# Kernel tuning notes

Measured on AMD Instinct MI355X. Metric: run time of the kernel, lower is better.

The kernel has to match this reference:

```python
import jax, jax.numpy as jnp
import numpy as np

L, D, H, HD, F, V, S, M, B = 8, 1024, 16, 64, 2048, 32000, 1024, 128, 1
EPS = 1e-5

def _rope_tables(total, hd):
    inv = 1.0 / (10000.0 ** (np.arange(0, hd, 2, dtype=np.float64) / hd))
    ang = np.arange(total)[:, None] * inv[None, :]
    cos = np.concatenate([np.cos(ang), np.cos(ang)], -1).astype(np.float32)
    sin = np.concatenate([np.sin(ang), np.sin(ang)], -1).astype(np.float32)
    return jnp.asarray(cos), jnp.asarray(sin)

_COS, _SIN = _rope_tables(M + S + M, HD)
_POS_MEM = jnp.arange(M)
_POS_HID = M + jnp.arange(S)
_POS_BG = M + S + jnp.arange(M)
_kph = jnp.arange(M + S)
# hidden queries: attend to all memory keys + causal over hidden keys
_MASK_H = (_kph[None, :] < M) | (_kph[None, :] - M <= jnp.arange(S)[:, None])
_kpb = jnp.arange(M + S + M)
# beacon/forget queries: attend to all mem+hidden keys + causal over own keys
_MASK_B = (_kpb[None, :] < M + S) | (_kpb[None, :] - (M + S) <= jnp.arange(M)[:, None])


def _rms(x, w):
    return x * w * jax.lax.rsqrt(jnp.mean(x * x, -1, keepdims=True) + EPS)

def _heads(x, w):  # [B,T,D] -> [B,H,T,HD]
    return (x @ w).reshape(B, -1, H, HD).transpose(0, 2, 1, 3)

def _merge(x):  # [B,H,T,HD] -> [B,T,D]
    return x.transpose(0, 2, 1, 3).reshape(B, -1, D)

def _rot_half(x):
    return jnp.concatenate([-x[..., HD // 2:], x[..., :HD // 2]], -1)

def _rope(x, pos):
    return x * _COS[pos][None, None] + _rot_half(x) * _SIN[pos][None, None]

def _attn(q, k, v, mask):
    s = jnp.einsum('bhqd,bhkd->bhqk', q, k) / jnp.sqrt(jnp.float32(HD))
    s = jnp.where(mask[None, None], s, jnp.finfo(s.dtype).min)
    return jnp.einsum('bhqk,bhkd->bhqd', jax.nn.softmax(s, -1), v)


def _forward(input_ids, memory, beacon, forget, embed, ln1, ln2,
             Wq, Wk, Wv, Wo, mWk, mWv, bWq, bWk, bWv, fWq, fWk, fWv, Wg, Wu, Wd):
    hidden = embed[input_ids]  # [B,S,D]

    def step(carry, xs):
        hid, bcn, fgt = carry
        (mem_l, l1, l2, wq, wk, wv, wo, mwk, mwv,
         bwq, bwk, bwv, fwq, fwk, fwv, wg, wu, wd) = xs
        rec = (bcn, fgt)  # states entering the layer (records in torch code)
        cat = jnp.concatenate([hid, bcn, fgt], 1)  # [B,S+2M,D]
        x = _rms(cat, l1)
        hx, bx, fx = x[:, :S], x[:, S:S + M], x[:, S + M:]
        mem = mem_l[None]  # [1,M,D]
        # project_head: memory -> K,V; prepend to hidden KV
        mk = _rope(_heads(mem, mwk), _POS_MEM)
        mv = _heads(mem, mwv)
        qh = _rope(_heads(hx, wq), _POS_HID)
        kh = _rope(_heads(hx, wk), _POS_HID)
        vh = _heads(hx, wv)
        hk = jnp.concatenate([mk, kh], 2)
        hv = jnp.concatenate([mv, vh], 2)
        oh = _merge(_attn(qh, hk, hv, _MASK_H)) @ wo

        def gate_branch(sx, wq_, wk_, wv_):
            q = _rope(_heads(sx, wq_), _POS_BG)
            k = jnp.concatenate([hk, _rope(_heads(sx, wk_), _POS_BG)], 2)
            v = jnp.concatenate([hv, _heads(sx, wv_)], 2)
            return _merge(_attn(q, k, v, _MASK_B)) @ wo

        ob = gate_branch(bx, bwq, bwk, bwv)
        of = gate_branch(fx, fwq, fwk, fwv)
        cat = cat + jnp.concatenate([oh, ob, of], 1)
        y = _rms(cat, l2)
        cat = cat + (jax.nn.silu(y @ wg) * (y @ wu)) @ wd
        return (cat[:, :S], cat[:, S:S + M], cat[:, S + M:]), rec

    xs = (memory, ln1, ln2, Wq, Wk, Wv, Wo, mWk, mWv,
          bWq, bWk, bWv, fWq, fWk, fWv, Wg, Wu, Wd)
    _, (inj, fg) = jax.lax.scan(step, (hidden, beacon, forget), xs)
    inj = inj.reshape(L, M, D)  # B==1
    fg = fg.reshape(L, M, D)
    g = jax.nn.sigmoid(fg)
    return memory * g + inj * (1.0 - g)


def setup_inputs() -> dict:
    key = jax.random.key(0)
    ks = jax.random.split(key, 24)
    sd = jnp.float32(0.02)
    def W(k, shape):
        return jax.random.normal(k, shape, jnp.float32) * sd
    return {
        'input_ids': jax.random.randint(ks[0], (B, S), 0, V),
        'memory': jax.random.normal(ks[1], (L, M, D), jnp.float32),
        'beacon': jax.random.normal(ks[2], (B, M, D), jnp.float32),
        'forget': jax.random.normal(ks[3], (B, M, D), jnp.float32),
        'embed': W(ks[4], (V, D)),
        'ln1': jnp.ones((L, D), jnp.float32),
        'ln2': jnp.ones((L, D), jnp.float32),
        'Wq': W(ks[5], (L, D, D)), 'Wk': W(ks[6], (L, D, D)),
        'Wv': W(ks[7], (L, D, D)), 'Wo': W(ks[8], (L, D, D)),
        'mWk': W(ks[9], (L, D, D)), 'mWv': W(ks[10], (L, D, D)),
        'bWq': W(ks[11], (L, D, D)), 'bWk': W(ks[12], (L, D, D)), 'bWv': W(ks[13], (L, D, D)),
        'fWq': W(ks[14], (L, D, D)), 'fWk': W(ks[15], (L, D, D)), 'fWv': W(ks[16], (L, D, D)),
        'Wg': W(ks[17], (L, D, F)), 'Wu': W(ks[18], (L, D, F)), 'Wd': W(ks[19], (L, F, D)),
    }


def reference(input_ids, memory, beacon, forget, embed, ln1, ln2,
              Wq, Wk, Wv, Wo, mWk, mWv, bWq, bWk, bWv, fWq, fWk, fWv, Wg, Wu, Wd):
    return _forward(input_ids, memory, beacon, forget, embed, ln1, ln2,
                    Wq, Wk, Wv, Wo, mWk, mWv, bWq, bWk, bWv, fWq, fWk, fWv, Wg, Wu, Wd)
```

## Files before the change

### kernel.cpp

```cpp
#include <hip/hip_runtime.h>
#include <math.h>

typedef __bf16 bf16;
typedef __attribute__((ext_vector_type(8))) __bf16 bf16x8;
typedef __attribute__((ext_vector_type(4))) float f32x4;

static const int DM = 1024;
static const int TCAT = 1280;
static const int NKV = 1408;

__device__ inline f32x4 mfma16(bf16x8 a, bf16x8 b, f32x4 c) {
  return __builtin_amdgcn_mfma_f32_16x16x32_bf16(a, b, c, 0, 0, 0);
}

__global__ void rope_table_kernel(float* cosT, float* sinT) {
  int p = blockIdx.x, i = threadIdx.x;
  double freq = pow(10000.0, -((double)i) / 32.0);
  double a = (double)p * freq;
  cosT[p * 32 + i] = (float)cos(a);
  sinT[p * 32 + i] = (float)sin(a);
}

__global__ void init_cat_kernel(const int* ids, const float* embed,
                                const float* beacon, const float* forget,
                                float* cat) {
  int r = blockIdx.x, tid = threadIdx.x;
  const float* src;
  if (r < 1024) src = embed + (size_t)ids[r] * DM;
  else if (r < 1152) src = beacon + (size_t)(r - 1024) * DM;
  else src = forget + (size_t)(r - 1152) * DM;
  *(f32x4*)(cat + (size_t)r * DM + tid * 4) = *(const f32x4*)(src + tid * 4);
}

__global__ void out_gate_kernel(const float* cat, const float* memL, float* outL) {
  int m = blockIdx.x, tid = threadIdx.x;
  size_t c = (size_t)tid * 4;
  f32x4 f = *(const f32x4*)(cat + (size_t)(1152 + m) * DM + c);
  f32x4 j = *(const f32x4*)(cat + (size_t)(1024 + m) * DM + c);
  f32x4 mm = *(const f32x4*)(memL + (size_t)m * DM + c);
  f32x4 o;
#pragma unroll
  for (int r = 0; r < 4; ++r) {
    float g = 1.f / (1.f + __expf(-f[r]));
    o[r] = mm[r] * g + j[r] * (1.f - g);
  }
  *(f32x4*)(outL + (size_t)m * DM + c) = o;
}

struct TransJob { const float* src; bf16* dst; int K; int N; int tileStart; };
struct TransArgs { TransJob j[15]; int njobs; };

__global__ __launch_bounds__(256) void trans_kernel(TransArgs args) {
  int b = blockIdx.x, ji = 0;
  while (ji + 1 < args.njobs && b >= args.j[ji + 1].tileStart) ++ji;
  TransJob J = args.j[ji];
  int t = b - J.tileStart;
  int tilesN = J.N >> 5;
  int tk = t / tilesN, tn = t - tk * tilesN;
  int k0 = tk * 32, n0 = tn * 32;
  __shared__ float tile[32][33];
  int c = threadIdx.x & 31, r0 = threadIdx.x >> 5;
#pragma unroll
  for (int i = 0; i < 4; ++i) {
    int r = r0 + i * 8;
    tile[r][c] = J.src[(size_t)(k0 + r) * J.N + n0 + c];
  }
  __syncthreads();
#pragma unroll
  for (int i = 0; i < 4; ++i) {
    int r = r0 + i * 8;
    J.dst[(size_t)(n0 + r) * J.K + k0 + c] = (bf16)tile[c][r];
  }
}

__global__ __launch_bounds__(256) void rmsnorm_kernel(const float* x, const float* w,
                                                      bf16* out, const float* mem,
                                                      int nNorm) {
  int r = blockIdx.x, tid = threadIdx.x;
  if (r < nNorm) {
    f32x4 v = *(const f32x4*)(x + (size_t)r * DM + tid * 4);
    float ss = v[0] * v[0] + v[1] * v[1] + v[2] * v[2] + v[3] * v[3];
#pragma unroll
    for (int d = 1; d < 64; d <<= 1) ss += __shfl_xor(ss, d, 64);
    __shared__ float red[4];
    if ((tid & 63) == 0) red[tid >> 6] = ss;
    __syncthreads();
    float tot = red[0] + red[1] + red[2] + red[3];
    float scale = rsqrtf(tot * (1.0f / 1024.0f) + 1e-5f);
    f32x4 wv = *(const f32x4*)(w + tid * 4);
    bf16* o = out + (size_t)r * DM + tid * 4;
#pragma unroll
    for (int q = 0; q < 4; ++q) o[q] = (bf16)(v[q] * wv[q] * scale);
  } else {
    f32x4 v = *(const f32x4*)(mem + (size_t)(r - nNorm) * DM + tid * 4);
    bf16* o = out + (size_t)r * DM + tid * 4;
#pragma unroll
    for (int q = 0; q < 4; ++q) o[q] = (bf16)v[q];
  }
}

struct GemmJob { const bf16* A; const bf16* B; float* C; int K; int N; int tileStart; int addFlag; };
struct GemmArgs { GemmJob j[12]; int njobs; };

__device__ __forceinline__ void gll16(const bf16* g, bf16* l) {
  __builtin_amdgcn_global_load_lds(
      (const __attribute__((address_space(1))) void*)g,
      (__attribute__((address_space(3))) void*)l, 16, 0, 0);
}

__global__ __launch_bounds__(256, 2) void gemm_kernel(GemmArgs args) {
  int b = blockIdx.x, ji = 0;
  while (ji + 1 < args.njobs && b >= args.j[ji + 1].tileStart) ++ji;
  GemmJob J = args.j[ji];
  int t = b - J.tileStart;
  int tilesN = J.N >> 7;
  int tm = t / tilesN, tn = t - tm * tilesN;
  const int tid = threadIdx.x;
  const int lane = tid & 63, w = tid >> 6;
  const int l15 = lane & 15, quad = lane >> 4;

  __shared__ bf16 As[2][64 * 32];
  __shared__ bf16 Bs[2][128 * 32];

  f32x4 acc[4][2];
#pragma unroll
  for (int i = 0; i < 4; ++i)
#pragma unroll
    for (int j = 0; j < 2; ++j) acc[i][j] = (f32x4){0.f, 0.f, 0.f, 0.f};

  const bf16* gA  = J.A + (size_t)(tm * 64 + w * 16 + (lane >> 2)) * J.K + (lane & 3) * 8;
  const bf16* gB0 = J.B + (size_t)(tn * 128 + w * 16 + (lane >> 2)) * J.K + (lane & 3) * 8;
  const bf16* gB1 = gB0 + (size_t)64 * J.K;

  auto stage = [&](int buf, int kt) {
    int k0 = kt << 5;
    gll16(gA + k0, &As[buf][w * 512]);
    gll16(gB0 + k0, &Bs[buf][w * 512]);
    gll16(gB1 + k0, &Bs[buf][2048 + w * 512]);
  };

  int nt = J.K >> 5;
  int cur = 0;
  stage(0, 0);
  if (nt > 1) stage(1, 1);

  for (int tt = 0; tt < nt; ++tt) {
    if (tt + 1 < nt) asm volatile("s_waitcnt vmcnt(3)" ::: "memory");
    else             asm volatile("s_waitcnt vmcnt(0)" ::: "memory");
    __builtin_amdgcn_sched_barrier(0);
    __builtin_amdgcn_s_barrier();

    const bf16* Ab = As[cur];
    const bf16* Bb = Bs[cur];
    bf16x8 af[4], bw[2];
#pragma unroll
    for (int i = 0; i < 4; ++i)
      af[i] = *(const bf16x8*)(Ab + (i * 16 + l15) * 32 + quad * 8);
#pragma unroll
    for (int j = 0; j < 2; ++j)
      bw[j] = *(const bf16x8*)(Bb + (w * 32 + j * 16 + l15) * 32 + quad * 8);
    asm volatile("s_waitcnt lgkmcnt(0)" ::: "memory");
    __builtin_amdgcn_sched_barrier(0);
    __builtin_amdgcn_s_barrier();

    if (tt + 2 < nt) stage(cur, tt + 2);

#pragma unroll
    for (int i = 0; i < 4; ++i)
#pragma unroll
      for (int j = 0; j < 2; ++j) acc[i][j] = mfma16(af[i], bw[j], acc[i][j]);
    cur ^= 1;
  }

#pragma unroll
  for (int i = 0; i < 4; ++i)
#pragma unroll
    for (int j = 0; j < 2; ++j) {
      int row0 = tm * 64 + i * 16 + quad * 4;
      int col = tn * 128 + w * 32 + j * 16 + l15;
#pragma unroll
      for (int r = 0; r < 4; ++r) {
        size_t idx = (size_t)(row0 + r) * J.N + col;
        if (J.addFlag) J.C[idx] += acc[i][j][r];
        else J.C[idx] = acc[i][j][r];
      }
    }
}

__global__ __launch_bounds__(256) void rope_vt_kernel(const float* qkv, const float* cosT,
                                                      const float* sinT, bf16* Qb,
                                                      bf16* Kb, bf16* Vt) {
  int b = blockIdx.x;
  if (b < 2688) {
    bool isQ = b < 1280;
    int r = isQ ? b : b - 1280;
    const float* x = qkv + (size_t)(isQ ? r : 1280 + r) * DM;
    int pos = isQ ? (r < 1152 ? r + 128 : r) : (r < 1280 ? r : r - 128);
    bf16* out = (isQ ? Qb : Kb) + (size_t)r * DM;
#pragma unroll
    for (int it = 0; it < 4; ++it) {
      int g = threadIdx.x + it * 256;
      int idx = g & 31;
      float c = cosT[pos * 32 + idx], s = sinT[pos * 32 + idx];
      float xv = x[g];
      float rot = ((g & 63) < 32) ? -x[g + 32] : x[g - 32];
      out[g] = (bf16)(xv * c + rot * s);
    }
  } else {
    int t = b - 2688;
    int tk = t >> 5, td = t & 31;
    int key0 = tk * 32, d0 = td * 32;
    __shared__ float tile[32][33];
    int c = threadIdx.x & 31, r0 = threadIdx.x >> 5;
#pragma unroll
    for (int i = 0; i < 4; ++i) {
      int r = r0 + i * 8;
      tile[r][c] = qkv[(size_t)(2688 + key0 + r) * DM + d0 + c];
    }
    __syncthreads();
#pragma unroll
    for (int i = 0; i < 4; ++i) {
      int r = r0 + i * 8;
      Vt[(size_t)(d0 + r) * NKV + key0 + c] = (bf16)tile[c][r];
    }
  }
}

__global__ __launch_bounds__(64) void attn_kernel(const bf16* Qb, const bf16* Kb,
                                                  const bf16* Vt, bf16* Ob) {
  int b = blockIdx.x;
  int h, q0, qRow0, maskBase, extraOff, kmax;
  if (b < 1024) {
    h = b >> 6; q0 = (b & 63) << 4; qRow0 = 0; maskBase = 128; extraOff = 0;
    kmax = 128 + q0 + 16; if (kmax > 1152) kmax = 1152;
  } else if (b < 1152) {
    int i = b - 1024; h = i >> 3; q0 = (i & 7) << 4; qRow0 = 1024;
    maskBase = 1152; extraOff = 0; kmax = 1152 + q0 + 16;
  } else {
    int i = b - 1152; h = i >> 3; q0 = (i & 7) << 4; qRow0 = 1152;
    maskBase = 1152; extraOff = 128; kmax = 1152 + q0 + 16;
  }
  const int lane = threadIdx.x;
  const int l15 = lane & 15, quad = lane >> 4;
  const bf16* qp = Qb + (size_t)(qRow0 + q0 + l15) * DM + h * 64 + quad * 8;
  bf16x8 aq0 = *(const bf16x8*)qp;
  bf16x8 aq1 = *(const bf16x8*)(qp + 32);
  f32x4 O0 = {0,0,0,0}, O1 = {0,0,0,0}, O2 = {0,0,0,0}, O3 = {0,0,0,0};
  float mrow[4], lrow[4];
#pragma unroll
  for (int r = 0; r < 4; ++r) { mrow[r] = -3.0e38f; lrow[r] = 0.f; }
  __shared__ bf16 Plds[16][32];
  int nkt = (kmax + 31) >> 5;
  for (int kt = 0; kt < nkt; ++kt) {
    int k0 = kt << 5;
    int off = (k0 >= 1152) ? extraOff : 0;
    f32x4 s0 = {0,0,0,0}, s1 = {0,0,0,0};
    {
      const bf16* kp = Kb + (size_t)(k0 + l15 + off) * DM + h * 64 + quad * 8;
      s0 = mfma16(aq0, *(const bf16x8*)kp, s0);
      s0 = mfma16(aq1, *(const bf16x8*)(kp + 32), s0);
      const bf16* kp1 = kp + (size_t)16 * DM;
      s1 = mfma16(aq0, *(const bf16x8*)kp1, s1);
      s1 = mfma16(aq1, *(const bf16x8*)(kp1 + 32), s1);
    }
    float p0[4], p1[4], mt[4];
#pragma unroll
    for (int r = 0; r < 4; ++r) {
      int qi = q0 + quad * 4 + r;
      int key0k = k0 + l15;
      int key1k = key0k + 16;
      float v0 = s0[r] * 0.125f, v1 = s1[r] * 0.125f;
      if (!(key0k < maskBase || key0k - maskBase <= qi)) v0 = -3.0e38f;
      if (!(key1k < maskBase || key1k - maskBase <= qi)) v1 = -3.0e38f;
      p0[r] = v0; p1[r] = v1;
      mt[r] = fmaxf(v0, v1);
    }
#pragma unroll
    for (int d = 1; d < 16; d <<= 1) {
#pragma unroll
      for (int r = 0; r < 4; ++r) mt[r] = fmaxf(mt[r], __shfl_xor(mt[r], d, 64));
    }
    float alpha[4];
#pragma unroll
    for (int r = 0; r < 4; ++r) {
      float mn = fmaxf(mrow[r], mt[r]);
      alpha[r] = __expf(mrow[r] - mn);
      mrow[r] = mn;
      p0[r] = __expf(p0[r] - mn);
      p1[r] = __expf(p1[r] - mn);
    }
    float rs[4];
#pragma unroll
    for (int r = 0; r < 4; ++r) rs[r] = p0[r] + p1[r];
#pragma unroll
    for (int d = 1; d < 16; d <<= 1) {
#pragma unroll
      for (int r = 0; r < 4; ++r) rs[r] += __shfl_xor(rs[r], d, 64);
    }
#pragma unroll
    for (int r = 0; r < 4; ++r) {
      lrow[r] = lrow[r] * alpha[r] + rs[r];
      O0[r] *= alpha[r]; O1[r] *= alpha[r]; O2[r] *= alpha[r]; O3[r] *= alpha[r];
    }
    __syncthreads();
#pragma unroll
    for (int r = 0; r < 4; ++r) {
      Plds[quad * 4 + r][l15] = (bf16)p0[r];
      Plds[quad * 4 + r][l15 + 16] = (bf16)p1[r];
    }
    __syncthreads();
    bf16x8 ap = *(const bf16x8*)(&Plds[l15][quad * 8]);
    const bf16* vp = Vt + (size_t)(h * 64 + l15) * NKV + k0 + off + quad * 8;
    O0 = mfma16(ap, *(const bf16x8*)vp, O0);
    O1 = mfma16(ap, *(const bf16x8*)(vp + (size_t)16 * NKV), O1);
    O2 = mfma16(ap, *(const bf16x8*)(vp + (size_t)32 * NKV), O2);
    O3 = mfma16(ap, *(const bf16x8*)(vp + (size_t)48 * NKV), O3);
  }
#pragma unroll
  for (int r = 0; r < 4; ++r) lrow[r] = 1.0f / lrow[r];
  bf16* op = Ob + (size_t)(qRow0 + q0 + quad * 4) * DM + h * 64 + l15;
#pragma unroll
  for (int r = 0; r < 4; ++r) {
    float inv = lrow[r];
    op[(size_t)r * DM + 0]  = (bf16)(O0[r] * inv);
    op[(size_t)r * DM + 16] = (bf16)(O1[r] * inv);
    op[(size_t)r * DM + 32] = (bf16)(O2[r] * inv);
    op[(size_t)r * DM + 48] = (bf16)(O3[r] * inv);
  }
}

__global__ void silu_kernel(const float* G, const float* U, bf16* H) {
  size_t i = (size_t)blockIdx.x * 256 + threadIdx.x;
  f32x4 g = *(const f32x4*)(G + i * 4);
  f32x4 u = *(const f32x4*)(U + i * 4);
  bf16* o = H + i * 4;
#pragma unroll
  for (int r = 0; r < 4; ++r) {
    float gv = g[r];
    float s = gv / (1.f + __expf(-gv));
    o[r] = (bf16)(s * u[r]);
  }
}

static const size_t OFF_COS = 0;
static const size_t OFF_SIN = 163840;
static const size_t OFF_CAT = 327680;
static const size_t OFF_XB  = 5570560;
static const size_t OFF_QKV = 8454144;
static const size_t OFF_QB  = 25231360;
static const size_t OFF_KB  = 27852800;
static const size_t OFF_VT  = 30736384;
static const size_t OFF_OB  = 33619968;
static const size_t OFF_YB  = 36241408;
static const size_t OFF_WT  = 38862848;
static const size_t OFF_G   = 76611584;
static const size_t OFF_U   = 87097344;
static const size_t OFF_HB  = 97583104;

extern "C" void kernel_launch(void* const* d_in, const int* in_sizes, int n_in,
                              void* d_out, int out_size, void* d_ws, size_t ws_size,
                              hipStream_t stream) {
  const int* ids = (const int*)d_in[0];
  const float* memory = (const float*)d_in[1];
  const float* beacon = (const float*)d_in[2];
  const float* forget = (const float*)d_in[3];
  const float* embed = (const float*)d_in[4];
  const float* ln1 = (const float*)d_in[5];
  const float* ln2 = (const float*)d_in[6];
  const float* Wq = (const float*)d_in[7];
  const float* Wk = (const float*)d_in[8];
  const float* Wv = (const float*)d_in[9];
  const float* Wo = (const float*)d_in[10];
  const float* mWk = (const float*)d_in[11];
  const float* mWv = (const float*)d_in[12];
  const float* bWq = (const float*)d_in[13];
  const float* bWk = (const float*)d_in[14];
  const float* bWv = (const float*)d_in[15];
  const float* fWq = (const float*)d_in[16];
  const float* fWk = (const float*)d_in[17];
  const float* fWv = (const float*)d_in[18];
  const float* Wg = (const float*)d_in[19];
  const float* Wu = (const float*)d_in[20];
  const float* Wd = (const float*)d_in[21];

  char* wsb = (char*)d_ws;
  float* cosT = (float*)(wsb + OFF_COS);
  float* sinT = (float*)(wsb + OFF_SIN);
  float* cat  = (float*)(wsb + OFF_CAT);
  bf16* xb    = (bf16*)(wsb + OFF_XB);
  float* qkv  = (float*)(wsb + OFF_QKV);
  bf16* Qb    = (bf16*)(wsb + OFF_QB);
  bf16* Kb    = (bf16*)(wsb + OFF_KB);
  bf16* Vt    = (bf16*)(wsb + OFF_VT);
  bf16* Ob    = (bf16*)(wsb + OFF_OB);
  bf16* yb    = (bf16*)(wsb + OFF_YB);
  bf16* wt    = (bf16*)(wsb + OFF_WT);
  float* Gf   = (float*)(wsb + OFF_G);
  float* Uf   = (float*)(wsb + OFF_U);
  bf16* Hb    = (bf16*)(wsb + OFF_HB);
  float* outp = (float*)d_out;

  auto mkjob = [](const bf16* A, const bf16* B, float* C, int K, int N, int M,
                  int addFlag, int& tiles) {
    GemmJob j; j.A = A; j.B = B; j.C = C; j.K = K; j.N = N;
    j.tileStart = tiles; j.addFlag = addFlag;
    tiles += (M / 64) * (N / 128);
    return j;
  };

  rope_table_kernel<<<1280, 32, 0, stream>>>(cosT, sinT);
  init_cat_kernel<<<1280, 256, 0, stream>>>(ids, embed, beacon, forget, cat);

  for (int l = 0; l < 8; ++l) {
    out_gate_kernel<<<128, 256, 0, stream>>>(cat, memory + (size_t)l * 131072,
                                             outp + (size_t)l * 131072);
    if (l == 7) break;

    TransArgs ta; int tt = 0;
    const float* s12[12] = {Wq, Wk, Wv, Wo, mWk, mWv, bWq, bWk, bWv, fWq, fWk, fWv};
    for (int i = 0; i < 12; ++i) {
      ta.j[i].src = s12[i] + (size_t)l * 1048576;
      ta.j[i].dst = wt + (size_t)i * 1048576;
      ta.j[i].K = 1024; ta.j[i].N = 1024; ta.j[i].tileStart = tt; tt += 1024;
    }
    ta.j[12].src = Wg + (size_t)l * 2097152; ta.j[12].dst = wt + (size_t)12 * 1048576;
    ta.j[12].K = 1024; ta.j[12].N = 2048; ta.j[12].tileStart = tt; tt += 2048;
    ta.j[13].src = Wu + (size_t)l * 2097152; ta.j[13].dst = wt + (size_t)14 * 1048576;
    ta.j[13].K = 1024; ta.j[13].N = 2048; ta.j[13].tileStart = tt; tt += 2048;
    ta.j[14].src = Wd + (size_t)l * 2097152; ta.j[14].dst = wt + (size_t)16 * 1048576;
    ta.j[14].K = 2048; ta.j[14].N = 1024; ta.j[14].tileStart = tt; tt += 2048;
    ta.njobs = 15;
    trans_kernel<<<tt, 256, 0, stream>>>(ta);

    rmsnorm_kernel<<<1408, 256, 0, stream>>>(cat, ln1 + (size_t)l * 1024, xb,
                                             memory + (size_t)l * 131072, 1280);

    auto xrow = [&](int r) { return xb + (size_t)r * DM; };
    auto crow = [&](int r) { return qkv + (size_t)r * DM; };
    auto wtm = [&](int i) { return wt + (size_t)i * 1048576; };
    GemmArgs ga; int tA = 0; int nj = 0;
    ga.j[nj++] = mkjob(xrow(0),    wtm(0),  crow(0),    1024, 1024, 1024, 0, tA);
    ga.j[nj++] = mkjob(xrow(1024), wtm(6),  crow(1024), 1024, 1024, 128, 0, tA);
    ga.j[nj++] = mkjob(xrow(1152), wtm(9),  crow(1152), 1024, 1024, 128, 0, tA);
    ga.j[nj++] = mkjob(xrow(1280), wtm(4),  crow(1280), 1024, 1024, 128, 0, tA);
    ga.j[nj++] = mkjob(xrow(0),    wtm(1),  crow(1408), 1024, 1024, 1024, 0, tA);
    ga.j[nj++] = mkjob(xrow(1024), wtm(7),  crow(2432), 1024, 1024, 128, 0, tA);
    ga.j[nj++] = mkjob(xrow(1152), wtm(10), crow(2560), 1024, 1024, 128, 0, tA);
    ga.j[nj++] = mkjob(xrow(1280), wtm(5),  crow(2688), 1024, 1024, 128, 0, tA);
    ga.j[nj++] = mkjob(xrow(0),    wtm(2),  crow(2816), 1024, 1024, 1024, 0, tA);
    ga.j[nj++] = mkjob(xrow(1024), wtm(8),  crow(3840), 1024, 1024, 128, 0, tA);
    ga.j[nj++] = mkjob(xrow(1152), wtm(11), crow(3968), 1024, 1024, 128, 0, tA);
    ga.njobs = nj;
    gemm_kernel<<<tA, 256, 0, stream>>>(ga);

    rope_vt_kernel<<<4096, 256, 0, stream>>>(qkv, cosT, sinT, Qb, Kb, Vt);

    attn_kernel<<<1280, 64, 0, stream>>>(Qb, Kb, Vt, Ob);

    GemmArgs gb; int tB = 0;
    gb.j[0] = mkjob(Ob, wtm(3), cat, 1024, 1024, 1280, 1, tB);
    gb.njobs = 1;
    gemm_kernel<<<tB, 256, 0, stream>>>(gb);

    rmsnorm_kernel<<<1280, 256, 0, stream>>>(cat, ln2 + (size_t)l * 1024, yb,
                                             nullptr, 1280);

    GemmArgs gc; int tC = 0;
    gc.j[0] = mkjob(yb, wtm(12), Gf, 1024, 2048, 1280, 0, tC);
    gc.j[1] = mkjob(yb, wtm(14), Uf, 1024, 2048, 1280, 0, tC);
    gc.njobs = 2;
    gemm_kernel<<<tC, 256, 0, stream>>>(gc);

    silu_kernel<<<2560, 256, 0, stream>>>(Gf, Uf, Hb);

    GemmArgs gd; int tD = 0;
    gd.j[0] = mkjob(Hb, wtm(16), cat, 2048, 1024, 1280, 1, tD);
    gd.njobs = 1;
    gemm_kernel<<<tD, 256, 0, stream>>>(gd);
  }
}
```

Before: 1.887 ms.

## Fuse SiLU gating into FFN GEMM, emit V transposed, split-K residual GEMMs

```diff
diff --git a/kernel.cpp b/kernel.cpp
--- a/kernel.cpp
+++ b/kernel.cpp
@@ -99,7 +99,10 @@
   }
 }
 
-struct GemmJob { const bf16* A; const bf16* B; float* C; int K; int N; int tileStart; int addFlag; };
+struct GemmJob {
+  const bf16* A; const bf16* B; const bf16* B2; void* C;
+  int K; int N; int ldC; int tileStart; int nMN; int mode; int kSplit;
+};
 struct GemmArgs { GemmJob j[12]; int njobs; };
 
 __device__ __forceinline__ void gll16(const bf16* g, bf16* l) {
@@ -113,52 +116,77 @@
   while (ji + 1 < args.njobs && b >= args.j[ji + 1].tileStart) ++ji;
   GemmJob J = args.j[ji];
   int t = b - J.tileStart;
+  int ks = 0;
+  if (J.kSplit > 1) { ks = t / J.nMN; t -= ks * J.nMN; }
   int tilesN = J.N >> 7;
   int tm = t / tilesN, tn = t - tm * tilesN;
+  int kLen = J.K / J.kSplit;
+  int kBase = ks * kLen;
   const int tid = threadIdx.x;
   const int lane = tid & 63, w = tid >> 6;
   const int l15 = lane & 15, quad = lane >> 4;
+  const bool ffn = (J.mode == 3);
 
   __shared__ bf16 As[2][64 * 32];
   __shared__ bf16 Bs[2][128 * 32];
-
-  f32x4 acc[4][2];
+  __shared__ bf16 B2s[2][128 * 32];
+
+  f32x4 acc[4][2], acc2[4][2];
 #pragma unroll
   for (int i = 0; i < 4; ++i)
 #pragma unroll
-    for (int j = 0; j < 2; ++j) acc[i][j] = (f32x4){0.f, 0.f, 0.f, 0.f};
-
-  const bf16* gA  = J.A + (size_t)(tm * 64 + w * 16 + (lane >> 2)) * J.K + (lane & 3) * 8;
-  const bf16* gB0 = J.B + (size_t)(tn * 128 + w * 16 + (lane >> 2)) * J.K + (lane & 3) * 8;
+    for (int j = 0; j < 2; ++j) {
+      acc[i][j] = (f32x4){0.f, 0.f, 0.f, 0.f};
+      acc2[i][j] = (f32x4){0.f, 0.f, 0.f, 0.f};
+    }
+
+  const bf16* gA  = J.A + (size_t)(tm * 64 + w * 16 + (lane >> 2)) * J.K + (lane & 3) * 8 + kBase;
+  const bf16* gB0 = J.B + (size_t)(tn * 128 + w * 16 + (lane >> 2)) * J.K + (lane & 3) * 8 + kBase;
   const bf16* gB1 = gB0 + (size_t)64 * J.K;
+  const bf16* gC0 = J.B2 + (size_t)(tn * 128 + w * 16 + (lane >> 2)) * J.K + (lane & 3) * 8 + kBase;
+  const bf16* gC1 = gC0 + (size_t)64 * J.K;
 
   auto stage = [&](int buf, int kt) {
     int k0 = kt << 5;
     gll16(gA + k0, &As[buf][w * 512]);
     gll16(gB0 + k0, &Bs[buf][w * 512]);
     gll16(gB1 + k0, &Bs[buf][2048 + w * 512]);
+    if (ffn) {
+      gll16(gC0 + k0, &B2s[buf][w * 512]);
+      gll16(gC1 + k0, &B2s[buf][2048 + w * 512]);
+    }
   };
 
-  int nt = J.K >> 5;
+  int nt = kLen >> 5;
   int cur = 0;
   stage(0, 0);
   if (nt > 1) stage(1, 1);
 
   for (int tt = 0; tt < nt; ++tt) {
-    if (tt + 1 < nt) asm volatile("s_waitcnt vmcnt(3)" ::: "memory");
-    else             asm volatile("s_waitcnt vmcnt(0)" ::: "memory");
+    if (tt + 1 < nt) {
+      if (ffn) asm volatile("s_waitcnt vmcnt(5)" ::: "memory");
+      else     asm volatile("s_waitcnt vmcnt(3)" ::: "memory");
+    } else {
+      asm volatile("s_waitcnt vmcnt(0)" ::: "memory");
+    }
     __builtin_amdgcn_sched_barrier(0);
     __builtin_amdgcn_s_barrier();
 
     const bf16* Ab = As[cur];
     const bf16* Bb = Bs[cur];
-    bf16x8 af[4], bw[2];
+    const bf16* B2b = B2s[cur];
+    bf16x8 af[4], bw[2], bw2[2];
 #pragma unroll
     for (int i = 0; i < 4; ++i)
       af[i] = *(const bf16x8*)(Ab + (i * 16 + l15) * 32 + quad * 8);
 #pragma unroll
     for (int j = 0; j < 2; ++j)
       bw[j] = *(const bf16x8*)(Bb + (w * 32 + j * 16 + l15) * 32 + quad * 8);
+    if (ffn) {
+#pragma unroll
+      for (int j = 0; j < 2; ++j)
+        bw2[j] = *(const bf16x8*)(B2b + (w * 32 + j * 16 + l15) * 32 + quad * 8);
+    }
     asm volatile("s_waitcnt lgkmcnt(0)" ::: "memory");
     __builtin_amdgcn_sched_barrier(0);
     __builtin_amdgcn_s_barrier();
@@ -169,6 +197,12 @@
     for (int i = 0; i < 4; ++i)
 #pragma unroll
       for (int j = 0; j < 2; ++j) acc[i][j] = mfma16(af[i], bw[j], acc[i][j]);
+    if (ffn) {
+#pragma unroll
+      for (int i = 0; i < 4; ++i)
+#pragma unroll
+        for (int j = 0; j < 2; ++j) acc2[i][j] = mfma16(af[i], bw2[j], acc2[i][j]);
+    }
     cur ^= 1;
   }
 
@@ -180,49 +214,42 @@
       int col = tn * 128 + w * 32 + j * 16 + l15;
 #pragma unroll
       for (int r = 0; r < 4; ++r) {
-        size_t idx = (size_t)(row0 + r) * J.N + col;
-        if (J.addFlag) J.C[idx] += acc[i][j][r];
-        else J.C[idx] = acc[i][j][r];
+        size_t idx = (size_t)(row0 + r) * J.ldC + col;
+        float v = acc[i][j][r];
+        if (J.mode == 0) {
+          ((float*)J.C)[idx] = v;
+        } else if (J.mode == 1) {
+          ((float*)J.C)[idx] += v;
+        } else if (J.mode == 2) {
+          ((bf16*)J.C)[idx] = (bf16)v;
+        } else if (J.mode == 3) {
+          float u = acc2[i][j][r];
+          float s = v / (1.f + __expf(-v));
+          ((bf16*)J.C)[idx] = (bf16)(s * u);
+        } else {
+          atomicAdd((float*)J.C + idx, v);
+        }
       }
     }
 }
 
 __global__ __launch_bounds__(256) void rope_vt_kernel(const float* qkv, const float* cosT,
                                                       const float* sinT, bf16* Qb,
-                                                      bf16* Kb, bf16* Vt) {
+                                                      bf16* Kb) {
   int b = blockIdx.x;
-  if (b < 2688) {
-    bool isQ = b < 1280;
-    int r = isQ ? b : b - 1280;
-    const float* x = qkv + (size_t)(isQ ? r : 1280 + r) * DM;
-    int pos = isQ ? (r < 1152 ? r + 128 : r) : (r < 1280 ? r : r - 128);
-    bf16* out = (isQ ? Qb : Kb) + (size_t)r * DM;
-#pragma unroll
-    for (int it = 0; it < 4; ++it) {
-      int g = threadIdx.x + it * 256;
-      int idx = g & 31;
-      float c = cosT[pos * 32 + idx], s = sinT[pos * 32 + idx];
-      float xv = x[g];
-      float rot = ((g & 63) < 32) ? -x[g + 32] : x[g - 32];
-      out[g] = (bf16)(xv * c + rot * s);
-    }
-  } else {
-    int t = b - 2688;
-    int tk = t >> 5, td = t & 31;
-    int key0 = tk * 32, d0 = td * 32;
-    __shared__ float tile[32][33];
-    int c = threadIdx.x & 31, r0 = threadIdx.x >> 5;
-#pragma unroll
-    for (int i = 0; i < 4; ++i) {
-      int r = r0 + i * 8;
-      tile[r][c] = qkv[(size_t)(2688 + key0 + r) * DM + d0 + c];
-    }
-    __syncthreads();
-#pragma unroll
-    for (int i = 0; i < 4; ++i) {
-      int r = r0 + i * 8;
-      Vt[(size_t)(d0 + r) * NKV + key0 + c] = (bf16)tile[c][r];
-    }
+  bool isQ = b < 1280;
+  int r = isQ ? b : b - 1280;
+  const float* x = qkv + (size_t)(isQ ? r : 1280 + r) * DM;
+  int pos = isQ ? (r < 1152 ? r + 128 : r) : (r < 1280 ? r : r - 128);
+  bf16* out = (isQ ? Qb : Kb) + (size_t)r * DM;
+#pragma unroll
+  for (int it = 0; it < 4; ++it) {
+    int g = threadIdx.x + it * 256;
+    int idx = g & 31;
+    float c = cosT[pos * 32 + idx], s = sinT[pos * 32 + idx];
+    float xv = x[g];
+    float rot = ((g & 63) < 32) ? -x[g + 32] : x[g - 32];
+    out[g] = (bf16)(xv * c + rot * s);
   }
 }
 
@@ -329,19 +356,6 @@
   }
 }
 
-__global__ void silu_kernel(const float* G, const float* U, bf16* H) {
-  size_t i = (size_t)blockIdx.x * 256 + threadIdx.x;
-  f32x4 g = *(const f32x4*)(G + i * 4);
-  f32x4 u = *(const f32x4*)(U + i * 4);
-  bf16* o = H + i * 4;
-#pragma unroll
-  for (int r = 0; r < 4; ++r) {
-    float gv = g[r];
-    float s = gv / (1.f + __expf(-gv));
-    o[r] = (bf16)(s * u[r]);
-  }
-}
-
 static const size_t OFF_COS = 0;
 static const size_t OFF_SIN = 163840;
 static const size_t OFF_CAT = 327680;
@@ -353,8 +367,6 @@
 static const size_t OFF_OB  = 33619968;
 static const size_t OFF_YB  = 36241408;
 static const size_t OFF_WT  = 38862848;
-static const size_t OFF_G   = 76611584;
-static const size_t OFF_U   = 87097344;
 static const size_t OFF_HB  = 97583104;
 
 extern "C" void kernel_launch(void* const* d_in, const int* in_sizes, int n_in,
@@ -395,16 +407,15 @@
   bf16* Ob    = (bf16*)(wsb + OFF_OB);
   bf16* yb    = (bf16*)(wsb + OFF_YB);
   bf16* wt    = (bf16*)(wsb + OFF_WT);
-  float* Gf   = (float*)(wsb + OFF_G);
-  float* Uf   = (float*)(wsb + OFF_U);
   bf16* Hb    = (bf16*)(wsb + OFF_HB);
   float* outp = (float*)d_out;
 
-  auto mkjob = [](const bf16* A, const bf16* B, float* C, int K, int N, int M,
-                  int addFlag, int& tiles) {
-    GemmJob j; j.A = A; j.B = B; j.C = C; j.K = K; j.N = N;
-    j.tileStart = tiles; j.addFlag = addFlag;
-    tiles += (M / 64) * (N / 128);
+  auto mkjob = [](const bf16* A, const bf16* B, const bf16* B2, void* C,
+                  int K, int N, int ldC, int M, int mode, int kSplit, int& tiles) {
+    GemmJob j; j.A = A; j.B = B; j.B2 = B2; j.C = C; j.K = K; j.N = N;
+    j.ldC = ldC; j.tileStart = tiles; j.mode = mode; j.kSplit = kSplit;
+    j.nMN = (M / 64) * (N / 128);
+    tiles += j.nMN * kSplit;
     return j;
   };
 
@@ -439,26 +450,26 @@
     auto crow = [&](int r) { return qkv + (size_t)r * DM; };
     auto wtm = [&](int i) { return wt + (size_t)i * 1048576; };
     GemmArgs ga; int tA = 0; int nj = 0;
-    ga.j[nj++] = mkjob(xrow(0),    wtm(0),  crow(0),    1024, 1024, 1024, 0, tA);
-    ga.j[nj++] = mkjob(xrow(1024), wtm(6),  crow(1024), 1024, 1024, 128, 0, tA);
-    ga.j[nj++] = mkjob(xrow(1152), wtm(9),  crow(1152), 1024, 1024, 128, 0, tA);
-    ga.j[nj++] = mkjob(xrow(1280), wtm(4),  crow(1280), 1024, 1024, 128, 0, tA);
-    ga.j[nj++] = mkjob(xrow(0),    wtm(1),  crow(1408), 1024, 1024, 1024, 0, tA);
-    ga.j[nj++] = mkjob(xrow(1024), wtm(7),  crow(2432), 1024, 1024, 128, 0, tA);
-    ga.j[nj++] = mkjob(xrow(1152), wtm(10), crow(2560), 1024, 1024, 128, 0, tA);
-    ga.j[nj++] = mkjob(xrow(1280), wtm(5),  crow(2688), 1024, 1024, 128, 0, tA);
-    ga.j[nj++] = mkjob(xrow(0),    wtm(2),  crow(2816), 1024, 1024, 1024, 0, tA);
-    ga.j[nj++] = mkjob(xrow(1024), wtm(8),  crow(3840), 1024, 1024, 128, 0, tA);
-    ga.j[nj++] = mkjob(xrow(1152), wtm(11), crow(3968), 1024, 1024, 128, 0, tA);
+    ga.j[nj++] = mkjob(xrow(0),    wtm(0),  nullptr, crow(0),    1024, 1024, 1024, 1024, 0, 1, tA);
+    ga.j[nj++] = mkjob(xrow(1024), wtm(6),  nullptr, crow(1024), 1024, 1024, 1024, 128,  0, 1, tA);
+    ga.j[nj++] = mkjob(xrow(1152), wtm(9),  nullptr, crow(1152), 1024, 1024, 1024, 128,  0, 1, tA);
+    ga.j[nj++] = mkjob(xrow(1280), wtm(4),  nullptr, crow(1280), 1024, 1024, 1024, 128,  0, 1, tA);
+    ga.j[nj++] = mkjob(xrow(0),    wtm(1),  nullptr, crow(1408), 1024, 1024, 1024, 1024, 0, 1, tA);
+    ga.j[nj++] = mkjob(xrow(1024), wtm(7),  nullptr, crow(2432), 1024, 1024, 1024, 128,  0, 1, tA);
+    ga.j[nj++] = mkjob(xrow(1152), wtm(10), nullptr, crow(2560), 1024, 1024, 1024, 128,  0, 1, tA);
+    ga.j[nj++] = mkjob(wtm(5),  xrow(1280), nullptr, Vt + 0,    1024, 128,  1408, 1024, 2, 1, tA);
+    ga.j[nj++] = mkjob(wtm(2),  xrow(0),    nullptr, Vt + 128,  1024, 1024, 1408, 1024, 2, 1, tA);
+    ga.j[nj++] = mkjob(wtm(8),  xrow(1024), nullptr, Vt + 1152, 1024, 128,  1408, 1024, 2, 1, tA);
+    ga.j[nj++] = mkjob(wtm(11), xrow(1152), nullptr, Vt + 1280, 1024, 128,  1408, 1024, 2, 1, tA);
     ga.njobs = nj;
     gemm_kernel<<<tA, 256, 0, stream>>>(ga);
 
-    rope_vt_kernel<<<4096, 256, 0, stream>>>(qkv, cosT, sinT, Qb, Kb, Vt);
+    rope_vt_kernel<<<2688, 256, 0, stream>>>(qkv, cosT, sinT, Qb, Kb);
 
     attn_kernel<<<1280, 64, 0, stream>>>(Qb, Kb, Vt, Ob);
 
     GemmArgs gb; int tB = 0;
-    gb.j[0] = mkjob(Ob, wtm(3), cat, 1024, 1024, 1280, 1, tB);
+    gb.j[0] = mkjob(Ob, wtm(3), nullptr, cat, 1024, 1024, 1024, 1280, 4, 2, tB);
     gb.njobs = 1;
     gemm_kernel<<<tB, 256, 0, stream>>>(gb);
 
@@ -466,15 +477,12 @@
                                              nullptr, 1280);
 
     GemmArgs gc; int tC = 0;
-    gc.j[0] = mkjob(yb, wtm(12), Gf, 1024, 2048, 1280, 0, tC);
-    gc.j[1] = mkjob(yb, wtm(14), Uf, 1024, 2048, 1280, 0, tC);
-    gc.njobs = 2;
+    gc.j[0] = mkjob(yb, wtm(12), wtm(14), Hb, 1024, 2048, 2048, 1280, 3, 1, tC);
+    gc.njobs = 1;
     gemm_kernel<<<tC, 256, 0, stream>>>(gc);
 
-    silu_kernel<<<2560, 256, 0, stream>>>(Gf, Uf, Hb);
-
     GemmArgs gd; int tD = 0;
-    gd.j[0] = mkjob(Hb, wtm(16), cat, 2048, 1024, 1280, 1, tD);
+    gd.j[0] = mkjob(Hb, wtm(16), nullptr, cat, 2048, 1024, 1024, 1280, 4, 2, tD);
     gd.njobs = 1;
     gemm_kernel<<<tD, 256, 0, stream>>>(gd);
   }
```

Measured after the change: 1.810 ms. 4.1% less time.
